# Kernel optimization log

Measured on AMD Instinct MI355X. Metric: run time of the kernel, lower is better.

Reference implementation:

```python
import jax, jax.numpy as jnp
from jax import lax
import numpy as np

T, B, I, H = 365, 2048, 9, 50


def setup_inputs() -> dict:
    key = jax.random.key(0)
    ks = jax.random.split(key, 12)
    s = 0.1
    return {
        "x": jax.random.normal(ks[0], (T, B, I), dtype=jnp.float32),
        "w_ih0": jax.random.normal(ks[1], (4 * H, I), dtype=jnp.float32) * s,
        "w_hh0": jax.random.normal(ks[2], (4 * H, H), dtype=jnp.float32) * s,
        "b_ih0": jax.random.normal(ks[3], (4 * H,), dtype=jnp.float32) * s,
        "b_hh0": jax.random.normal(ks[4], (4 * H,), dtype=jnp.float32) * s,
        "w_ih1": jax.random.normal(ks[5], (4 * H, H), dtype=jnp.float32) * s,
        "w_hh1": jax.random.normal(ks[6], (4 * H, H), dtype=jnp.float32) * s,
        "b_ih1": jax.random.normal(ks[7], (4 * H,), dtype=jnp.float32) * s,
        "b_hh1": jax.random.normal(ks[8], (4 * H,), dtype=jnp.float32) * s,
        "fc_w": jax.random.normal(ks[9], (1, H), dtype=jnp.float32) * s,
        "fc_b": jax.random.normal(ks[10], (1,), dtype=jnp.float32) * s,
    }


def _lstm_layer(x, w_ih, w_hh, b_ih, b_hh):
    # x: [T, B, in]; PyTorch gate order: i, f, g, o
    Bq = x.shape[1]
    Hh = w_hh.shape[1]
    # precompute input projections for all timesteps (one big GEMM)
    x_proj = jnp.einsum('tbi,gi->tbg', x, w_ih) + b_ih + b_hh  # [T, B, 4H]

    def step(carry, xp):
        h, c = carry
        gates = xp + h @ w_hh.T  # [B, 4H]
        i, f, g, o = jnp.split(gates, 4, axis=-1)
        i = jax.nn.sigmoid(i)
        f = jax.nn.sigmoid(f)
        g = jnp.tanh(g)
        o = jax.nn.sigmoid(o)
        c = f * c + i * g
        h = o * jnp.tanh(c)
        return (h, c), h

    h0 = jnp.zeros((Bq, Hh), dtype=x.dtype)
    _, hs = lax.scan(step, (h0, h0), x_proj)
    return hs  # [T, B, H]


def reference(x, w_ih0, w_hh0, b_ih0, b_hh0, w_ih1, w_hh1, b_ih1, b_hh1, fc_w, fc_b):
    h1 = _lstm_layer(x, w_ih0, w_hh0, b_ih0, b_hh0)
    h2 = _lstm_layer(h1, w_ih1, w_hh1, b_ih1, b_hh1)
    out = jnp.einsum('tbh,oh->tbo', h2, fc_w) + fc_b  # [T, B, 1]
    return out
```

## Files before the change

kernel.cpp:

```cpp
#include <hip/hip_runtime.h>

#define T_STEPS 365
#define BATCH   2048
#define INP     9
#define HID     50
#define MB      16
#define NBLK    (BATCH/MB)
#define NT      512
#define NWC     7
#define NTILES  13
#define L2E     1.4426950408889634f

typedef __attribute__((ext_vector_type(8))) short short8;
typedef __attribute__((ext_vector_type(4))) float float4v;

__device__ __forceinline__ unsigned f2bf(float v) {
    unsigned u = __builtin_bit_cast(unsigned, v);
    return (u + 0x7FFFu + ((u >> 16) & 1u)) >> 16;
}

#define PHASE_BARRIER() do {                                  \
    asm volatile("s_waitcnt lgkmcnt(0)" ::: "memory");        \
    __builtin_amdgcn_s_barrier();                             \
    __builtin_amdgcn_sched_barrier(0);                        \
} while (0)

__device__ __forceinline__ int tx_off(int m, int k) {
    return ((k >> 3) * 128) + m * 8 + (k & 7);
}

__device__ __forceinline__ float cell_(float a0, float a1, float a2, float a3,
                                       float& c) {
    const float Ei = __builtin_amdgcn_exp2f(a0);
    const float Ef = __builtin_amdgcn_exp2f(a1);
    const float Eg = __builtin_amdgcn_exp2f(a2);
    const float Eo = __builtin_amdgcn_exp2f(a3);
    const float ig = (1.f - Eg) * __builtin_amdgcn_rcpf((1.f + Ei) * (1.f + Eg));
    c = __builtin_amdgcn_rcpf(1.f + Ef) * c + ig;
    const float Ec = __builtin_amdgcn_exp2f(c * (-2.f * L2E));
    return (1.f - Ec) * __builtin_amdgcn_rcpf((1.f + Eo) * (1.f + Ec));
}

__global__ __launch_bounds__(NT, 2)
void lstm_fuse8(const float* __restrict__ x,
                const float* __restrict__ w_ih0, const float* __restrict__ w_hh0,
                const float* __restrict__ b_ih0, const float* __restrict__ b_hh0,
                const float* __restrict__ w_ih1, const float* __restrict__ w_hh1,
                const float* __restrict__ b_ih1, const float* __restrict__ b_hh1,
                const float* __restrict__ fc_w, const float* __restrict__ fc_b,
                float* __restrict__ out)
{
    __shared__ __align__(16) unsigned short HX[2][2048];

    const int tid  = threadIdx.x;
    const int w    = tid >> 6;
    const int lid  = tid & 63;
    const int mcol = lid & 15;
    const int kgrp = lid >> 4;
    const int kb8  = kgrp * 8;
    const int b0   = blockIdx.x * MB;
    const bool cw  = (w < NWC);

    short8 wk0[2][2], wk1[2][2], wk2[2][2];
    float  bs0[2][4], bs1[2][4];
    float  cst0[2] = {0.f, 0.f}, cst1[2] = {0.f, 0.f};

    #pragma unroll
    for (int tt = 0; tt < 2; ++tt) {
        const int T  = w + NWC * tt;
        const bool tv = cw && (T < NTILES);
        const int r  = T * 16 + mcol;
        const bool rv = tv && (r < 4 * HID);
        const int u_r = r >> 2, g_r = r & 3;
        const int orig = g_r * HID + u_r;
        const float rsc = (g_r == 2) ? (-2.f * L2E) : (-L2E);
        const bool fcrow = tv && (T == 12) && (mcol == 8);
        #pragma unroll
        for (int q = 0; q < 2; ++q) {
            short8 a{}, b{}, c{};
            #pragma unroll
            for (int j = 0; j < 8; ++j) {
                const int k = q * 32 + kb8 + j;
                float v0 = 0.f, v1 = 0.f, v2 = 0.f;
                if (rv) {
                    if (k < HID) {
                        v0 = w_hh0[orig * HID + k] * rsc;
                        v1 = w_ih1[orig * HID + k] * rsc;
                        v2 = w_hh1[orig * HID + k] * rsc;
                    } else if (k < HID + INP) {
                        v0 = w_ih0[orig * INP + (k - HID)] * rsc;
                    }
                }
                if (fcrow) v2 = (k < HID) ? fc_w[k] : 0.f;
                a[j] = (short)f2bf(v0);
                b[j] = (short)f2bf(v1);
                c[j] = (short)f2bf(v2);
            }
            wk0[tt][q] = a; wk1[tt][q] = b; wk2[tt][q] = c;
        }
        #pragma unroll
        for (int rr = 0; rr < 4; ++rr) {
            const int row = T * 16 + kgrp * 4 + rr;
            const bool bv = tv && (row < 4 * HID);
            const int uu = row >> 2;
            const float bsc = (rr == 2) ? (-2.f * L2E) : (-L2E);
            bs0[tt][rr] = bv ? (b_ih0[rr * HID + uu] + b_hh0[rr * HID + uu]) * bsc : 0.f;
            bs1[tt][rr] = bv ? (b_ih1[rr * HID + uu] + b_hh1[rr * HID + uu]) * bsc : 0.f;
            if (tv && row == 4 * HID) bs1[tt][rr] = fc_b[0];
        }
    }

    const bool xact = (!cw) && (lid < 48);
    float xr[3] = {0.f, 0.f, 0.f};

    for (int i = tid; i < 2 * 2048; i += NT) (&HX[0][0])[i] = 0;
    __syncthreads();
    if (xact) {
        #pragma unroll
        for (int q = 0; q < 3; ++q) {
            const int xi = lid * 3 + q;
            if (xi < MB * INP) {
                const int m = xi / INP, j = xi - m * INP;
                HX[1][tx_off(m, HID + j)] =
                    (unsigned short)f2bf(x[(size_t)(b0 + m) * INP + j]);
                xr[q] = x[((size_t)BATCH + b0 + m) * INP + j];
            }
        }
    }
    __syncthreads();

    for (int ph = 0; ph <= T_STEPS + 1; ++ph) {
        const int cur = (ph + 1) & 1, nxt = ph & 1;

        if (cw) {
            const int base = mcol * 8;
            const short8 f0 = *(const short8*)&HX[cur][(kgrp)      * 128 + base];
            const short8 f1 = *(const short8*)&HX[cur][(4  + kgrp) * 128 + base];
            const short8 f2 = *(const short8*)&HX[cur][(8  + kgrp) * 128 + base];
            const short8 f3 = *(const short8*)&HX[cur][(12 + kgrp) * 128 + base];

            #pragma unroll
            for (int tt = 0; tt < 2; ++tt) {
                const int T = w + NWC * tt;
                if (T >= NTILES) continue;
                const int u = T * 4 + kgrp;

                if (ph < T_STEPS) {
                    float4v acc = {bs0[tt][0], bs0[tt][1], bs0[tt][2], bs0[tt][3]};
                    acc = __builtin_amdgcn_mfma_f32_16x16x32_bf16(wk0[tt][0], f0, acc, 0, 0, 0);
                    acc = __builtin_amdgcn_mfma_f32_16x16x32_bf16(wk0[tt][1], f1, acc, 0, 0, 0);
                    const float h0v = cell_(acc[0], acc[1], acc[2], acc[3], cst0[tt]);
                    if (u < HID) HX[nxt][tx_off(mcol, u)] = (unsigned short)f2bf(h0v);
                }

                if (ph >= 1) {
                    float4v accA = {bs1[tt][0], bs1[tt][1], bs1[tt][2], bs1[tt][3]};
                    float4v accB = {0.f, 0.f, 0.f, 0.f};
                    accA = __builtin_amdgcn_mfma_f32_16x16x32_bf16(wk1[tt][0], f0, accA, 0, 0, 0);
                    accB = __builtin_amdgcn_mfma_f32_16x16x32_bf16(wk2[tt][0], f2, accB, 0, 0, 0);
                    accA = __builtin_amdgcn_mfma_f32_16x16x32_bf16(wk1[tt][1], f1, accA, 0, 0, 0);
                    accB = __builtin_amdgcn_mfma_f32_16x16x32_bf16(wk2[tt][1], f3, accB, 0, 0, 0);
                    const float a0 = accA[0] + accB[0];
                    const float a1 = accA[1] + accB[1];
                    const float a2 = accA[2] + accB[2];
                    const float a3 = accA[3] + accB[3];
                    if (T == 12 && kgrp == 2 && ph >= 2)
                        out[(size_t)(ph - 2) * BATCH + b0 + mcol] = a0;
                    if (ph <= T_STEPS) {
                        const float h1v = cell_(a0, a1, a2, a3, cst1[tt]);
                        if (u < HID) HX[nxt][tx_off(mcol, 64 + u)] = (unsigned short)f2bf(h1v);
                    }
                }
            }
        } else if (xact) {
            #pragma unroll
            for (int q = 0; q < 3; ++q) {
                const int xi = lid * 3 + q;
                if (xi < MB * INP) {
                    const int m = xi / INP, j = xi - m * INP;
                    float xn = 0.f;
                    if (ph + 2 < T_STEPS)
                        xn = x[((size_t)(ph + 2) * BATCH + b0 + m) * INP + j];
                    if (ph + 1 < T_STEPS)
                        HX[nxt][tx_off(m, HID + j)] = (unsigned short)f2bf(xr[q]);
                    xr[q] = xn;
                }
            }
        }
        PHASE_BARRIER();
    }
}

extern "C" void kernel_launch(void* const* d_in, const int* in_sizes, int n_in,
                              void* d_out, int out_size, void* d_ws, size_t ws_size,
                              hipStream_t stream) {
    const float* x     = (const float*)d_in[0];
    const float* w_ih0 = (const float*)d_in[1];
    const float* w_hh0 = (const float*)d_in[2];
    const float* b_ih0 = (const float*)d_in[3];
    const float* b_hh0 = (const float*)d_in[4];
    const float* w_ih1 = (const float*)d_in[5];
    const float* w_hh1 = (const float*)d_in[6];
    const float* b_ih1 = (const float*)d_in[7];
    const float* b_hh1 = (const float*)d_in[8];
    const float* fc_w  = (const float*)d_in[9];
    const float* fc_b  = (const float*)d_in[10];
    float* out = (float*)d_out;

    lstm_fuse8<<<dim3(NBLK), dim3(NT), 0, stream>>>(
        x, w_ih0, w_hh0, b_ih0, b_hh0,
        w_ih1, w_hh1, b_ih1, b_hh1, fc_w, fc_b, out);
}
```

Before: 335.6 us.

## Replace per-step workgroup barriers with LDS producer/consumer flag counters

Removes the full workgroup barrier at the end of each timestep. In its place, each of the two double-buffered HX slots gets a pair of LDS counters, one for producers and one for consumers. A wave waits only until all eight waves have written the buffer it reads, and only until all readers have finished with the buffer it is about to overwrite. This lets waves drift apart and overlap compute, at the cost of spin-polling with s_sleep, atomic traffic, and subtle memory-ordering risk from relaxed atomics.

```diff
diff --git a/kernel.cpp b/kernel.cpp
--- a/kernel.cpp
+++ b/kernel.cpp
@@ -9,6 +9,7 @@
 #define NT      512
 #define NWC     7
 #define NTILES  13
+#define NWAVES  8
 #define L2E     1.4426950408889634f
 
 typedef __attribute__((ext_vector_type(8))) short short8;
@@ -18,12 +19,6 @@
     unsigned u = __builtin_bit_cast(unsigned, v);
     return (u + 0x7FFFu + ((u >> 16) & 1u)) >> 16;
 }
-
-#define PHASE_BARRIER() do {                                  \
-    asm volatile("s_waitcnt lgkmcnt(0)" ::: "memory");        \
-    __builtin_amdgcn_s_barrier();                             \
-    __builtin_amdgcn_sched_barrier(0);                        \
-} while (0)
 
 __device__ __forceinline__ int tx_off(int m, int k) {
     return ((k >> 3) * 128) + m * 8 + (k & 7);
@@ -41,8 +36,21 @@
     return (1.f - Ec) * __builtin_amdgcn_rcpf((1.f + Eo) * (1.f + Ec));
 }
 
+__device__ __forceinline__ void waitflag(unsigned* f, unsigned tgt) {
+    while (__hip_atomic_load(f, __ATOMIC_RELAXED, __HIP_MEMORY_SCOPE_WORKGROUP) < tgt)
+        __builtin_amdgcn_s_sleep(1);
+    asm volatile("" ::: "memory");
+    __builtin_amdgcn_sched_barrier(0);
+}
+__device__ __forceinline__ void bumpflag(unsigned* f, bool lead) {
+    asm volatile("s_waitcnt lgkmcnt(0)" ::: "memory");
+    if (lead)
+        __hip_atomic_fetch_add(f, 1u, __ATOMIC_RELAXED, __HIP_MEMORY_SCOPE_WORKGROUP);
+    __builtin_amdgcn_sched_barrier(0);
+}
+
 __global__ __launch_bounds__(NT, 2)
-void lstm_fuse8(const float* __restrict__ x,
+void lstm_flags(const float* __restrict__ x,
                 const float* __restrict__ w_ih0, const float* __restrict__ w_hh0,
                 const float* __restrict__ b_ih0, const float* __restrict__ b_hh0,
                 const float* __restrict__ w_ih1, const float* __restrict__ w_hh1,
@@ -51,6 +59,7 @@
                 float* __restrict__ out)
 {
     __shared__ __align__(16) unsigned short HX[2][2048];
+    __shared__ unsigned PROD[2], CONS[2];
 
     const int tid  = threadIdx.x;
     const int w    = tid >> 6;
@@ -60,6 +69,7 @@
     const int kb8  = kgrp * 8;
     const int b0   = blockIdx.x * MB;
     const bool cw  = (w < NWC);
+    const bool lead = (lid == 0);
 
     short8 wk0[2][2], wk1[2][2], wk2[2][2];
     float  bs0[2][4], bs1[2][4];
@@ -114,6 +124,7 @@
     float xr[3] = {0.f, 0.f, 0.f};
 
     for (int i = tid; i < 2 * 2048; i += NT) (&HX[0][0])[i] = 0;
+    if (tid < 2) { PROD[tid] = 0; CONS[tid] = 0; }
     __syncthreads();
     if (xact) {
         #pragma unroll
@@ -131,28 +142,29 @@
 
     for (int ph = 0; ph <= T_STEPS + 1; ++ph) {
         const int cur = (ph + 1) & 1, nxt = ph & 1;
+        const unsigned k8 = (unsigned)(NWAVES * ((ph + 1) >> 1));
 
         if (cw) {
+            waitflag(&PROD[cur], k8);
             const int base = mcol * 8;
             const short8 f0 = *(const short8*)&HX[cur][(kgrp)      * 128 + base];
             const short8 f1 = *(const short8*)&HX[cur][(4  + kgrp) * 128 + base];
             const short8 f2 = *(const short8*)&HX[cur][(8  + kgrp) * 128 + base];
             const short8 f3 = *(const short8*)&HX[cur][(12 + kgrp) * 128 + base];
-
+            bumpflag(&CONS[cur], lead);
+
+            float h0v[2] = {0.f, 0.f}, h1v[2] = {0.f, 0.f};
             #pragma unroll
             for (int tt = 0; tt < 2; ++tt) {
                 const int T = w + NWC * tt;
                 if (T >= NTILES) continue;
-                const int u = T * 4 + kgrp;
 
                 if (ph < T_STEPS) {
                     float4v acc = {bs0[tt][0], bs0[tt][1], bs0[tt][2], bs0[tt][3]};
                     acc = __builtin_amdgcn_mfma_f32_16x16x32_bf16(wk0[tt][0], f0, acc, 0, 0, 0);
                     acc = __builtin_amdgcn_mfma_f32_16x16x32_bf16(wk0[tt][1], f1, acc, 0, 0, 0);
-                    const float h0v = cell_(acc[0], acc[1], acc[2], acc[3], cst0[tt]);
-                    if (u < HID) HX[nxt][tx_off(mcol, u)] = (unsigned short)f2bf(h0v);
-                }
-
+                    h0v[tt] = cell_(acc[0], acc[1], acc[2], acc[3], cst0[tt]);
+                }
                 if (ph >= 1) {
                     float4v accA = {bs1[tt][0], bs1[tt][1], bs1[tt][2], bs1[tt][3]};
                     float4v accB = {0.f, 0.f, 0.f, 0.f};
@@ -166,28 +178,51 @@
                     const float a3 = accA[3] + accB[3];
                     if (T == 12 && kgrp == 2 && ph >= 2)
                         out[(size_t)(ph - 2) * BATCH + b0 + mcol] = a0;
-                    if (ph <= T_STEPS) {
-                        const float h1v = cell_(a0, a1, a2, a3, cst1[tt]);
-                        if (u < HID) HX[nxt][tx_off(mcol, 64 + u)] = (unsigned short)f2bf(h1v);
+                    if (ph <= T_STEPS)
+                        h1v[tt] = cell_(a0, a1, a2, a3, cst1[tt]);
+                }
+            }
+
+            waitflag(&CONS[nxt], k8);
+            #pragma unroll
+            for (int tt = 0; tt < 2; ++tt) {
+                const int T = w + NWC * tt;
+                if (T >= NTILES) continue;
+                const int u = T * 4 + kgrp;
+                if (ph < T_STEPS && u < HID)
+                    HX[nxt][tx_off(mcol, u)] = (unsigned short)f2bf(h0v[tt]);
+                if (ph >= 1 && ph <= T_STEPS && u < HID)
+                    HX[nxt][tx_off(mcol, 64 + u)] = (unsigned short)f2bf(h1v[tt]);
+            }
+            bumpflag(&PROD[nxt], lead);
+        } else {
+            bumpflag(&CONS[cur], lead);
+            float xn[3] = {0.f, 0.f, 0.f};
+            if (xact && ph + 2 < T_STEPS) {
+                #pragma unroll
+                for (int q = 0; q < 3; ++q) {
+                    const int xi = lid * 3 + q;
+                    if (xi < MB * INP) {
+                        const int m = xi / INP, j = xi - m * INP;
+                        xn[q] = x[((size_t)(ph + 2) * BATCH + b0 + m) * INP + j];
                     }
                 }
             }
-        } else if (xact) {
-            #pragma unroll
-            for (int q = 0; q < 3; ++q) {
-                const int xi = lid * 3 + q;
-                if (xi < MB * INP) {
-                    const int m = xi / INP, j = xi - m * INP;
-                    float xn = 0.f;
-                    if (ph + 2 < T_STEPS)
-                        xn = x[((size_t)(ph + 2) * BATCH + b0 + m) * INP + j];
-                    if (ph + 1 < T_STEPS)
+            waitflag(&CONS[nxt], k8);
+            if (xact && ph + 1 < T_STEPS) {
+                #pragma unroll
+                for (int q = 0; q < 3; ++q) {
+                    const int xi = lid * 3 + q;
+                    if (xi < MB * INP) {
+                        const int m = xi / INP, j = xi - m * INP;
                         HX[nxt][tx_off(m, HID + j)] = (unsigned short)f2bf(xr[q]);
-                    xr[q] = xn;
-                }
-            }
-        }
-        PHASE_BARRIER();
+                    }
+                }
+            }
+            #pragma unroll
+            for (int q = 0; q < 3; ++q) xr[q] = xn[q];
+            bumpflag(&PROD[nxt], lead);
+        }
     }
 }
 
@@ -207,7 +242,7 @@
     const float* fc_b  = (const float*)d_in[10];
     float* out = (float*)d_out;
 
-    lstm_fuse8<<<dim3(NBLK), dim3(NT), 0, stream>>>(
+    lstm_flags<<<dim3(NBLK), dim3(NT), 0, stream>>>(
         x, w_ih0, w_hh0, b_ih0, b_hh0,
         w_ih1, w_hh1, b_ih1, b_hh1, fc_w, fc_b, out);
 }
```

Measured after the change: 453.9 us. 35.2% more time.
